# Kernel tuning notes

Measured on AMD Instinct MI355X. Metric: run time of the kernel, lower is better.

## Reference

```python
import jax, jax.numpy as jnp
import numpy as np

EPS = 1e-5
STEPS = 4
MULTIPLIER = 4
CROP_SHIFT = 4  # deterministic stand-in for RandomCrop: translate by 4px


def _box_blur(x):
    # 3x3 box blur, reflect padding (kornia RandomBoxBlur default), shape-preserving
    H, W = x.shape[-2], x.shape[-1]
    xp = jnp.pad(x, ((0, 0), (0, 0), (1, 1), (1, 1)), mode='reflect')
    acc = xp[..., 0:H, 0:W]
    for i in range(3):
        for j in range(3):
            if i == 0 and j == 0:
                continue
            acc = acc + xp[..., i:i + H, j:j + W]
    return acc / 9.0


def _mixed_op(h, w):
    # weighted sum over the 7 DA_2D_PRIMITIVES (deterministic versions):
    # none, blur, invert, hflip, vflip, crop(translate), rotate(90 deg)
    return (w[0] * h
            + w[1] * _box_blur(h)
            + w[2] * (1.0 - h)
            + w[3] * jnp.flip(h, axis=-1)
            + w[4] * jnp.flip(h, axis=-2)
            + w[5] * jnp.roll(h, shift=(CROP_SHIFT, CROP_SHIFT), axis=(-2, -1))
            + w[6] * jnp.rot90(h, k=1, axes=(-2, -1)))


def _cell(s0, s1, weights):
    states = [s0, s1]
    offset = 0
    for i in range(STEPS):
        s = states[0] * 0.0
        for j, h in enumerate(states):
            s = s + _mixed_op(h, weights[offset + j])
        offset += len(states)
        states.append(s)
    return jnp.concatenate(states[-MULTIPLIER:], axis=1)


def setup_inputs() -> dict:
    key = jax.random.key(0)
    k1, k2, k3 = jax.random.split(key, 3)
    B, C, H, W = 16, 48, 128, 128
    return {
        'x': jax.random.normal(k1, (B, C, H, W), dtype=jnp.float32),
        'gamma': jnp.ones((C,), dtype=jnp.float32),
        'beta': jnp.zeros((C,), dtype=jnp.float32),
        'alphas_normal': 0.001 * jax.random.normal(k2, (14, 7), dtype=jnp.float32),
        'alphas_reduce': 0.001 * jax.random.normal(k3, (14, 7), dtype=jnp.float32),
    }


def reference(x, gamma, beta, alphas_normal, alphas_reduce):
    # stem: BatchNorm2d in training mode (batch statistics)
    mean = jnp.mean(x, axis=(0, 2, 3), keepdims=True)
    var = jnp.var(x, axis=(0, 2, 3), keepdims=True)
    s = (x - mean) * jax.lax.rsqrt(var + EPS)
    s = s * gamma[None, :, None, None] + beta[None, :, None, None]
    # layers=1: cell 0 is a reduction cell -> uses alphas_reduce
    w = jax.nn.softmax(alphas_reduce, axis=-1)  # [14 edges, 7 ops]
    return _cell(s, s, w)
```

## Files before the change

### kernel.cpp

```cpp
#include <hip/hip_runtime.h>
#include <math.h>

#define NCH 48
#define NB 16
#define PLANE 16384
#define NPLANES 768

#define WS_PSUM  0
#define WS_PSQ   768
#define WS_SCALE 1536
#define WS_SHIFT 1584
#define WS_TAB   1632
#define WS_CONST 1728

typedef _Float16 h2 __attribute__((ext_vector_type(2)));

__global__ __launch_bounds__(256) void stats_kernel(const float* __restrict__ x,
                                                    float* __restrict__ ws) {
  int p = blockIdx.x;
  int t = threadIdx.x;
  const float4* x4 = (const float4*)x + (size_t)p * 4096;
  float s = 0.f, q = 0.f;
  #pragma unroll
  for (int k = 0; k < 16; ++k) {
    float4 v = x4[k * 256 + t];
    s += v.x + v.y + v.z + v.w;
    q += v.x * v.x + v.y * v.y + v.z * v.z + v.w * v.w;
  }
  #pragma unroll
  for (int off = 32; off > 0; off >>= 1) {
    s += __shfl_xor(s, off, 64);
    q += __shfl_xor(q, off, 64);
  }
  __shared__ float red[8];
  int wid = t >> 6, lane = t & 63;
  if (lane == 0) { red[wid] = s; red[4 + wid] = q; }
  __syncthreads();
  if (t == 0) {
    ws[WS_PSUM + p] = red[0] + red[1] + red[2] + red[3];
    ws[WS_PSQ  + p] = red[4] + red[5] + red[6] + red[7];
  }
}

__global__ void prep_kernel(const float* __restrict__ gamma, const float* __restrict__ beta,
                            const float* __restrict__ alphas, float* __restrict__ ws) {
  int t = threadIdx.x;
  if (t < NCH) {
    float s = 0.f, q = 0.f;
    for (int b = 0; b < NB; ++b) {
      s += ws[WS_PSUM + b * NCH + t];
      q += ws[WS_PSQ  + b * NCH + t];
    }
    const float inv = 1.0f / ((float)NB * PLANE);
    float mean = s * inv;
    float var  = q * inv - mean * mean;
    float sc = gamma[t] * rsqrtf(var + 1e-5f);
    ws[WS_SCALE + t] = sc;
    ws[WS_SHIFT + t] = beta[t] - mean * sc;
  }
  if (t == 0) {
    float w[14][7];
    for (int r = 0; r < 14; ++r) {
      float m = -1e30f;
      for (int k = 0; k < 7; ++k) m = fmaxf(m, alphas[r * 7 + k]);
      float sum = 0.f;
      for (int k = 0; k < 7; ++k) { float e = expf(alphas[r * 7 + k] - m); w[r][k] = e; sum += e; }
      float is = 1.0f / sum;
      for (int k = 0; k < 7; ++k) w[r][k] *= is;
    }
    for (int i = 0; i < 96; ++i) ws[WS_TAB + i] = 0.f;
    for (int i = 0; i < 4;  ++i) ws[WS_CONST + i] = 0.f;
    const int map[14][2] = {
      {0,0},{0,0},
      {0,1},{0,1},{1,1},
      {0,2},{0,2},{1,2},{2,2},
      {0,3},{0,3},{1,3},{2,3},{3,3}
    };
    for (int r = 0; r < 14; ++r) {
      int p = map[r][0], tg = map[r][1];
      float* cf = ws + WS_TAB + (p * 4 + tg) * 6;
      cf[0] += w[r][0] - w[r][2];
      cf[1] += w[r][1] * (1.0f / 9.0f);
      cf[2] += w[r][3];
      cf[3] += w[r][4];
      cf[4] += w[r][5];
      cf[5] += w[r][6];
      ws[WS_CONST + tg] += w[r][2];
    }
  }
}


__device__ __forceinline__ float ldshw(const h2* L, int i, int j) {
  int q = ((j >> 2) & 31) ^ (i >> 2);
  h2 p = L[(i << 6) + ((j & 2) << 4) + q];
  return (j & 1) ? (float)p.y : (float)p.x;
}

#define RDQ(L, I, B, M) {                                                      \
  int q_ = (B) ^ ((I) >> 2);                                                   \
  h2 p0_ = (L)[((I) << 6) + q_];                                               \
  h2 p1_ = (L)[((I) << 6) + 32 + q_];                                          \
  M.x = (float)p0_.x; M.y = (float)p0_.y;                                      \
  M.z = (float)p1_.x; M.w = (float)p1_.y; }

#define WRQ(L, I, B, V) {                                                      \
  int q_ = (B) ^ ((I) >> 2);                                                   \
  h2 p0_, p1_;                                                                 \
  p0_.x = (_Float16)V.x; p0_.y = (_Float16)V.y;                                \
  p1_.x = (_Float16)V.z; p1_.y = (_Float16)V.w;                                \
  (L)[((I) << 6) + q_] = p0_;                                                  \
  (L)[((I) << 6) + 32 + q_] = p1_; }

#define HROW(h, m, lo, hi)                                                     \
  h.x = lo + m.x + m.y; h.y = m.x + m.y + m.z;                                 \
  h.z = m.y + m.z + m.w; h.w = m.z + m.w + hi;

#define FMA4(T, C, M)                                                          \
  T.x += (C) * M.x; T.y += (C) * M.y; T.z += (C) * M.z; T.w += (C) * M.w;

#define BLUR4(T, A, B, Cq)                                                     \
  T.x += c1 * (A.x + B.x + Cq.x); T.y += c1 * (A.y + B.y + Cq.y);              \
  T.z += c1 * (A.z + B.z + Cq.z); T.w += c1 * (A.w + B.w + Cq.w);

#define FLIPL(T, M)                                                            \
  T.x += c2 * M.w; T.y += c2 * M.z; T.z += c2 * M.y; T.w += c2 * M.x;

#define GATHER(L, OI, TYC) {                                                   \
  float4 m, hA, hB, hC; float lo, hi; int ri;                                  \
  ri = ((OI) == 0) ? 1 : (OI) - 1;                                             \
  RDQ(L, ri, tx, m) lo = ldshw(L, ri, cLo); hi = ldshw(L, ri, cHi);            \
  HROW(hA, m, lo, hi)                                                          \
  RDQ(L, (OI), tx, m) lo = ldshw(L, (OI), cLo); hi = ldshw(L, (OI), cHi);      \
  FMA4(T0, c0, m)                                                              \
  HROW(hB, m, lo, hi)                                                          \
  RDQ(L, (OI)+1, tx, m) lo = ldshw(L, (OI)+1, cLo); hi = ldshw(L, (OI)+1, cHi);\
  FMA4(T1, c0, m)                                                              \
  HROW(hC, m, lo, hi)                                                          \
  BLUR4(T0, hA, hB, hC)                                                        \
  RDQ(L, (OI)+2, tx, m) lo = ldshw(L, (OI)+2, cLo); hi = ldshw(L, (OI)+2, cHi);\
  FMA4(T1, 0.0f, m)                                            \
  FMA4(T2, c0, m)                                                              \
  HROW(hA, m, lo, hi)                                                          \
  BLUR4(T1, hB, hC, hA)                                                        \
  RDQ(L, (OI)+3, tx, m) lo = ldshw(L, (OI)+3, cLo); hi = ldshw(L, (OI)+3, cHi);\
  FMA4(T3, c0, m)                                                              \
  HROW(hB, m, lo, hi)                                                          \
  BLUR4(T2, hC, hA, hB)                                                        \
  ri = ((OI) == 124) ? 126 : (OI) + 4;                                         \
  RDQ(L, ri, tx, m) lo = ldshw(L, ri, cLo); hi = ldshw(L, ri, cHi);            \
  HROW(hC, m, lo, hi)                                                          \
  BLUR4(T3, hA, hB, hC)                                                        \
                                                                   \
  RDQ(L, (OI),   31 - tx, m) FLIPL(T0, m)                                      \
  RDQ(L, (OI)+1, 31 - tx, m) FLIPL(T1, m)                                      \
  RDQ(L, (OI)+2, 31 - tx, m) FLIPL(T2, m)                                      \
  RDQ(L, (OI)+3, 31 - tx, m) FLIPL(T3, m)                                      \
                                                                   \
  RDQ(L, 127 - (OI), tx, m) FMA4(T0, c3, m)                                    \
  RDQ(L, 126 - (OI), tx, m) FMA4(T1, c3, m)                                    \
  RDQ(L, 125 - (OI), tx, m) FMA4(T2, c3, m)                                    \
  RDQ(L, 124 - (OI), tx, m) FMA4(T3, c3, m)                                    \
                                                              \
  RDQ(L, ((OI) - 4) & 127, rc, m) FMA4(T0, c4, m)                              \
  RDQ(L, ((OI) - 3) & 127, rc, m) FMA4(T1, c4, m)                              \
  RDQ(L, ((OI) - 2) & 127, rc, m) FMA4(T2, c4, m)                              \
  RDQ(L, ((OI) - 1) & 127, rc, m) FMA4(T3, c4, m)                              \
                                     \
  RDQ(L, oj,     31 - (TYC), m)                                                \
  T0.x += c5 * m.w; T1.x += c5 * m.z; T2.x += c5 * m.y; T3.x += c5 * m.x;      \
  RDQ(L, oj + 1, 31 - (TYC), m)                                                \
  T0.y += c5 * m.w; T1.y += c5 * m.z; T2.y += c5 * m.y; T3.y += c5 * m.x;      \
  RDQ(L, oj + 2, 31 - (TYC), m)                                                \
  T0.z += c5 * m.w; T1.z += c5 * m.z; T2.z += c5 * m.y; T3.z += c5 * m.x;      \
  RDQ(L, oj + 3, 31 - (TYC), m)                                                \
  T0.w += c5 * m.w; T1.w += c5 * m.z; T2.w += c5 * m.y; T3.w += c5 * m.x;      \
}

#define LDCF(P, TG) {                                                          \
  const float* cfp = wsf + WS_TAB + ((P) * 4 + (TG)) * 6;                      \
  c0 = cfp[0]; c1 = cfp[1]; c2 = cfp[2]; c3 = cfp[3]; c4 = cfp[4]; c5 = cfp[5]; }

#define SETC(K) {                                                              \
  float cst = wsf[WS_CONST + (K)];                                             \
  T0.x = cst; T0.y = cst; T0.z = cst; T0.w = cst; T1 = T0; T2 = T0; T3 = T0; }

#define STAGE_BN(L, OI) {                                                      \
  float4 v;                                                                    \
  v = x4[((OI)+0)*32 + tx]; v.x = v.x*sc+sh; v.y = v.y*sc+sh; v.z = v.z*sc+sh; \
  v.w = v.w*sc+sh; WRQ(L, (OI)+0, tx, v)                                       \
  v = x4[((OI)+1)*32 + tx]; v.x = v.x*sc+sh; v.y = v.y*sc+sh; v.z = v.z*sc+sh; \
  v.w = v.w*sc+sh; WRQ(L, (OI)+1, tx, v)                                       \
  v = x4[((OI)+2)*32 + tx]; v.x = v.x*sc+sh; v.y = v.y*sc+sh; v.z = v.z*sc+sh; \
  v.w = v.w*sc+sh; WRQ(L, (OI)+2, tx, v)                                       \
  v = x4[((OI)+3)*32 + tx]; v.x = v.x*sc+sh; v.y = v.y*sc+sh; v.z = v.z*sc+sh; \
  v.w = v.w*sc+sh; WRQ(L, (OI)+3, tx, v) }

#define STAGE_OUT(L, TG, OI) {                                                 \
  float4 v;                                                                    \
  v = out4[(pbase + (TG)*NCH)*4096 + ((OI)+0)*32 + tx]; WRQ(L, (OI)+0, tx, v)  \
  v = out4[(pbase + (TG)*NCH)*4096 + ((OI)+1)*32 + tx]; WRQ(L, (OI)+1, tx, v)  \
  v = out4[(pbase + (TG)*NCH)*4096 + ((OI)+2)*32 + tx]; WRQ(L, (OI)+2, tx, v)  \
  v = out4[(pbase + (TG)*NCH)*4096 + ((OI)+3)*32 + tx]; WRQ(L, (OI)+3, tx, v) }

#define WRITEV(TG, OI) {                                                       \
  out4[(pbase + (TG)*NCH)*4096 + ((OI)+0)*32 + tx] = T0;                       \
  out4[(pbase + (TG)*NCH)*4096 + ((OI)+1)*32 + tx] = T1;                       \
  out4[(pbase + (TG)*NCH)*4096 + ((OI)+2)*32 + tx] = T2;                       \
  out4[(pbase + (TG)*NCH)*4096 + ((OI)+3)*32 + tx] = T3; }

#define LOADV(TG, OI) {                                                        \
  T0 = out4[(pbase + (TG)*NCH)*4096 + ((OI)+0)*32 + tx];                       \
  T1 = out4[(pbase + (TG)*NCH)*4096 + ((OI)+1)*32 + tx];                       \
  T2 = out4[(pbase + (TG)*NCH)*4096 + ((OI)+2)*32 + tx];                       \
  T3 = out4[(pbase + (TG)*NCH)*4096 + ((OI)+3)*32 + tx]; }

#define STASHV(L, OI) {                                                        \
  WRQ(L, (OI)+0, tx, T0) WRQ(L, (OI)+1, tx, T1)                                \
  WRQ(L, (OI)+2, tx, T2) WRQ(L, (OI)+3, tx, T3) }

__global__ __launch_bounds__(256, 1)
void main_kernel(const float* __restrict__ x,
                 const float* __restrict__ wsf, float* out)
{
  __shared__ h2 lds[2 * 8192];
  h2* h0 = lds;
  h2* h1 = lds + 8192;
  int bx = blockIdx.x;
  int b = bx / NCH, c = bx % NCH;
  int tid = threadIdx.x;
  int ty = tid >> 5, tx = tid & 31;
  int oj = tx << 2;
  int cLo = (tx == 0)  ? 1   : oj - 1;
  int cHi = (tx == 31) ? 126 : oj + 4;
  int rc  = (tx + 31) & 31;
  float4* out4 = (float4*)out;
  const size_t pbase = (size_t)b * 192 + c;
  const float4* x4 = (const float4*)x + (size_t)bx * 4096;
  float sc = wsf[WS_SCALE + c], sh = wsf[WS_SHIFT + c];

  float4 T0, T1, T2, T3;
  float c0, c1, c2, c3, c4, c5;

  #pragma unroll 1
  for (int k = 0; k < 4; ++k) {
    int oi = (ty + 8 * k) << 2;
    STAGE_BN(h0, oi);
  }
  __syncthreads();

  #pragma unroll 1
  for (int k = 0; k < 4; ++k) {
    int oi = (ty + 8 * k) << 2; int tyc = ty + 8 * k;
    SETC(0); LDCF(0, 0);
    GATHER(h0, oi, tyc);
    WRITEV(0, oi);
    STASHV(h1, oi);
  }
  __syncthreads();

  #pragma unroll 1
  for (int k = 0; k < 4; ++k) {
    int oi = (ty + 8 * k) << 2; int tyc = ty + 8 * k;
    SETC(1); LDCF(0, 1); GATHER(h0, oi, tyc);
             LDCF(1, 1); GATHER(h1, oi, tyc);
    WRITEV(1, oi);
    SETC(2); LDCF(0, 2); GATHER(h0, oi, tyc);
             LDCF(1, 2); GATHER(h1, oi, tyc);
    WRITEV(2, oi);
    SETC(3); LDCF(0, 3); GATHER(h0, oi, tyc);
             LDCF(1, 3); GATHER(h1, oi, tyc);
    WRITEV(3, oi);
  }
  __syncthreads();

  #pragma unroll 1
  for (int k = 0; k < 4; ++k) {
    int oi = (ty + 8 * k) << 2;
    STAGE_OUT(h0, 1, oi);
  }
  __syncthreads();

  #pragma unroll 1
  for (int k = 0; k < 4; ++k) {
    int oi = (ty + 8 * k) << 2; int tyc = ty + 8 * k;
    LOADV(2, oi); LDCF(2, 2); GATHER(h0, oi, tyc); WRITEV(2, oi);
    STASHV(h1, oi);
  }
  __syncthreads();

  #pragma unroll 1
  for (int k = 0; k < 4; ++k) {
    int oi = (ty + 8 * k) << 2; int tyc = ty + 8 * k;
    LOADV(3, oi);
    LDCF(2, 3); GATHER(h0, oi, tyc);
    LDCF(3, 3); GATHER(h1, oi, tyc);
    WRITEV(3, oi);
  }
}

extern "C" void kernel_launch(void* const* d_in, const int* in_sizes, int n_in,
                              void* d_out, int out_size, void* d_ws, size_t ws_size,
                              hipStream_t stream) {
  (void)in_sizes; (void)n_in; (void)out_size; (void)ws_size;
  const float* x     = (const float*)d_in[0];
  const float* gamma = (const float*)d_in[1];
  const float* beta  = (const float*)d_in[2];
  const float* a_red = (const float*)d_in[4];
  float* ws  = (float*)d_ws;
  float* out = (float*)d_out;

  stats_kernel<<<NPLANES, 256, 0, stream>>>(x, ws);
  prep_kernel<<<1, 64, 0, stream>>>(gamma, beta, a_red, ws);
  main_kernel<<<NPLANES, 256, 0, stream>>>(x, ws, out);
}
```

Baseline: 116.6 us.

## Share LDS gathers across three target states and hoist coefficient loads out of loops

The second phase used to gather from h0 and h1 once for each of the three target states. It now gathers once per source and accumulates into three register accumulators, each with its own coefficient set. This cuts LDS reads and fp16-to-float conversions in that phase to about a third. Coefficient loads from the workspace are hoisted out of the loops, and a redundant zero-FMA is removed. The cost is much higher register pressure: 12 float4 accumulators and 36 scalar coefficients, which risks spills under launch_bounds(256,1).

```diff
diff --git a/kernel.cpp b/kernel.cpp
--- a/kernel.cpp
+++ b/kernel.cpp
@@ -104,11 +104,11 @@
   M.x = (float)p0_.x; M.y = (float)p0_.y;                                      \
   M.z = (float)p1_.x; M.w = (float)p1_.y; }
 
-#define WRQ(L, I, B, V) {                                                      \
+#define WRQ(L, I, B, VV) {                                                     \
   int q_ = (B) ^ ((I) >> 2);                                                   \
   h2 p0_, p1_;                                                                 \
-  p0_.x = (_Float16)V.x; p0_.y = (_Float16)V.y;                                \
-  p1_.x = (_Float16)V.z; p1_.y = (_Float16)V.w;                                \
+  p0_.x = (_Float16)VV.x; p0_.y = (_Float16)VV.y;                              \
+  p1_.x = (_Float16)VV.z; p1_.y = (_Float16)VV.w;                              \
   (L)[((I) << 6) + q_] = p0_;                                                  \
   (L)[((I) << 6) + 32 + q_] = p1_; }
 
@@ -116,74 +116,73 @@
   h.x = lo + m.x + m.y; h.y = m.x + m.y + m.z;                                 \
   h.z = m.y + m.z + m.w; h.w = m.z + m.w + hi;
 
-#define FMA4(T, C, M)                                                          \
-  T.x += (C) * M.x; T.y += (C) * M.y; T.z += (C) * M.z; T.w += (C) * M.w;
-
-#define BLUR4(T, A, B, Cq)                                                     \
-  T.x += c1 * (A.x + B.x + Cq.x); T.y += c1 * (A.y + B.y + Cq.y);              \
-  T.z += c1 * (A.z + B.z + Cq.z); T.w += c1 * (A.w + B.w + Cq.w);
-
-#define FLIPL(T, M)                                                            \
-  T.x += c2 * M.w; T.y += c2 * M.z; T.z += c2 * M.y; T.w += c2 * M.x;
-
-#define GATHER(L, OI, TYC) {                                                   \
+#define FMA4A(ACC, R, OP, M) ACC(R,x,OP,M.x) ACC(R,y,OP,M.y) ACC(R,z,OP,M.z) ACC(R,w,OP,M.w)
+#define FLIPLA(ACC, R, M)    ACC(R,x,2,M.w) ACC(R,y,2,M.z) ACC(R,z,2,M.y) ACC(R,w,2,M.x)
+#define BLUR4A(ACC, R, Ah, Bh, Ch)                                             \
+  ACC(R,x,1,(Ah.x+Bh.x+Ch.x)) ACC(R,y,1,(Ah.y+Bh.y+Ch.y))                      \
+  ACC(R,z,1,(Ah.z+Bh.z+Ch.z)) ACC(R,w,1,(Ah.w+Bh.w+Ch.w))
+
+#define GATHER(L, OI, TYC, ACC) {                                              \
   float4 m, hA, hB, hC; float lo, hi; int ri;                                  \
   ri = ((OI) == 0) ? 1 : (OI) - 1;                                             \
   RDQ(L, ri, tx, m) lo = ldshw(L, ri, cLo); hi = ldshw(L, ri, cHi);            \
   HROW(hA, m, lo, hi)                                                          \
   RDQ(L, (OI), tx, m) lo = ldshw(L, (OI), cLo); hi = ldshw(L, (OI), cHi);      \
-  FMA4(T0, c0, m)                                                              \
+  FMA4A(ACC, 0, 0, m)                                                          \
   HROW(hB, m, lo, hi)                                                          \
   RDQ(L, (OI)+1, tx, m) lo = ldshw(L, (OI)+1, cLo); hi = ldshw(L, (OI)+1, cHi);\
-  FMA4(T1, c0, m)                                                              \
+  FMA4A(ACC, 1, 0, m)                                                          \
   HROW(hC, m, lo, hi)                                                          \
-  BLUR4(T0, hA, hB, hC)                                                        \
+  BLUR4A(ACC, 0, hA, hB, hC)                                                   \
   RDQ(L, (OI)+2, tx, m) lo = ldshw(L, (OI)+2, cLo); hi = ldshw(L, (OI)+2, cHi);\
-  FMA4(T1, 0.0f, m)                                            \
-  FMA4(T2, c0, m)                                                              \
+  FMA4A(ACC, 2, 0, m)                                                          \
   HROW(hA, m, lo, hi)                                                          \
-  BLUR4(T1, hB, hC, hA)                                                        \
+  BLUR4A(ACC, 1, hB, hC, hA)                                                   \
   RDQ(L, (OI)+3, tx, m) lo = ldshw(L, (OI)+3, cLo); hi = ldshw(L, (OI)+3, cHi);\
-  FMA4(T3, c0, m)                                                              \
+  FMA4A(ACC, 3, 0, m)                                                          \
   HROW(hB, m, lo, hi)                                                          \
-  BLUR4(T2, hC, hA, hB)                                                        \
+  BLUR4A(ACC, 2, hC, hA, hB)                                                   \
   ri = ((OI) == 124) ? 126 : (OI) + 4;                                         \
   RDQ(L, ri, tx, m) lo = ldshw(L, ri, cLo); hi = ldshw(L, ri, cHi);            \
   HROW(hC, m, lo, hi)                                                          \
-  BLUR4(T3, hA, hB, hC)                                                        \
+  BLUR4A(ACC, 3, hA, hB, hC)                                                   \
                                                                    \
-  RDQ(L, (OI),   31 - tx, m) FLIPL(T0, m)                                      \
-  RDQ(L, (OI)+1, 31 - tx, m) FLIPL(T1, m)                                      \
-  RDQ(L, (OI)+2, 31 - tx, m) FLIPL(T2, m)                                      \
-  RDQ(L, (OI)+3, 31 - tx, m) FLIPL(T3, m)                                      \
+  RDQ(L, (OI),   31 - tx, m) FLIPLA(ACC, 0, m)                                 \
+  RDQ(L, (OI)+1, 31 - tx, m) FLIPLA(ACC, 1, m)                                 \
+  RDQ(L, (OI)+2, 31 - tx, m) FLIPLA(ACC, 2, m)                                 \
+  RDQ(L, (OI)+3, 31 - tx, m) FLIPLA(ACC, 3, m)                                 \
                                                                    \
-  RDQ(L, 127 - (OI), tx, m) FMA4(T0, c3, m)                                    \
-  RDQ(L, 126 - (OI), tx, m) FMA4(T1, c3, m)                                    \
-  RDQ(L, 125 - (OI), tx, m) FMA4(T2, c3, m)                                    \
-  RDQ(L, 124 - (OI), tx, m) FMA4(T3, c3, m)                                    \
+  RDQ(L, 127 - (OI), tx, m) FMA4A(ACC, 0, 3, m)                                \
+  RDQ(L, 126 - (OI), tx, m) FMA4A(ACC, 1, 3, m)                                \
+  RDQ(L, 125 - (OI), tx, m) FMA4A(ACC, 2, 3, m)                                \
+  RDQ(L, 124 - (OI), tx, m) FMA4A(ACC, 3, 3, m)                                \
                                                               \
-  RDQ(L, ((OI) - 4) & 127, rc, m) FMA4(T0, c4, m)                              \
-  RDQ(L, ((OI) - 3) & 127, rc, m) FMA4(T1, c4, m)                              \
-  RDQ(L, ((OI) - 2) & 127, rc, m) FMA4(T2, c4, m)                              \
-  RDQ(L, ((OI) - 1) & 127, rc, m) FMA4(T3, c4, m)                              \
+  RDQ(L, ((OI) - 4) & 127, rc, m) FMA4A(ACC, 0, 4, m)                          \
+  RDQ(L, ((OI) - 3) & 127, rc, m) FMA4A(ACC, 1, 4, m)                          \
+  RDQ(L, ((OI) - 2) & 127, rc, m) FMA4A(ACC, 2, 4, m)                          \
+  RDQ(L, ((OI) - 1) & 127, rc, m) FMA4A(ACC, 3, 4, m)                          \
                                      \
   RDQ(L, oj,     31 - (TYC), m)                                                \
-  T0.x += c5 * m.w; T1.x += c5 * m.z; T2.x += c5 * m.y; T3.x += c5 * m.x;      \
+  ACC(0,x,5,m.w) ACC(1,x,5,m.z) ACC(2,x,5,m.y) ACC(3,x,5,m.x)                  \
   RDQ(L, oj + 1, 31 - (TYC), m)                                                \
-  T0.y += c5 * m.w; T1.y += c5 * m.z; T2.y += c5 * m.y; T3.y += c5 * m.x;      \
+  ACC(0,y,5,m.w) ACC(1,y,5,m.z) ACC(2,y,5,m.y) ACC(3,y,5,m.x)                  \
   RDQ(L, oj + 2, 31 - (TYC), m)                                                \
-  T0.z += c5 * m.w; T1.z += c5 * m.z; T2.z += c5 * m.y; T3.z += c5 * m.x;      \
+  ACC(0,z,5,m.w) ACC(1,z,5,m.z) ACC(2,z,5,m.y) ACC(3,z,5,m.x)                  \
   RDQ(L, oj + 3, 31 - (TYC), m)                                                \
-  T0.w += c5 * m.w; T1.w += c5 * m.z; T2.w += c5 * m.y; T3.w += c5 * m.x;      \
-}
-
-#define LDCF(P, TG) {                                                          \
-  const float* cfp = wsf + WS_TAB + ((P) * 4 + (TG)) * 6;                      \
-  c0 = cfp[0]; c1 = cfp[1]; c2 = cfp[2]; c3 = cfp[3]; c4 = cfp[4]; c5 = cfp[5]; }
-
-#define SETC(K) {                                                              \
-  float cst = wsf[WS_CONST + (K)];                                             \
-  T0.x = cst; T0.y = cst; T0.z = cst; T0.w = cst; T1 = T0; T2 = T0; T3 = T0; }
+  ACC(0,w,5,m.w) ACC(1,w,5,m.z) ACC(2,w,5,m.y) ACC(3,w,5,m.x)                  \
+}
+
+#define ACC_T(R,Cc,OP,VAL)  T##R.Cc += cA##OP * (VAL);
+#define ACC_TB(R,Cc,OP,VAL) T##R.Cc += cB##OP * (VAL);
+#define ACC_3A(R,Cc,OP,VAL) { float v_=(VAL); T##R.Cc += cA##OP*v_; U##R.Cc += cB##OP*v_; W##R.Cc += cC##OP*v_; }
+#define ACC_3B(R,Cc,OP,VAL) { float v_=(VAL); T##R.Cc += cD##OP*v_; U##R.Cc += cE##OP*v_; W##R.Cc += cF##OP*v_; }
+
+#define LDCFS(PRE, P, TG) {                                                    \
+  const float* cfp_ = wsf + WS_TAB + ((P) * 4 + (TG)) * 6;                     \
+  PRE##0 = cfp_[0]; PRE##1 = cfp_[1]; PRE##2 = cfp_[2];                        \
+  PRE##3 = cfp_[3]; PRE##4 = cfp_[4]; PRE##5 = cfp_[5]; }
+
+#define SET4(A, VV) { A##0 = VV; A##1 = VV; A##2 = VV; A##3 = VV; }
 
 #define STAGE_BN(L, OI) {                                                      \
   float4 v;                                                                    \
@@ -203,21 +202,21 @@
   v = out4[(pbase + (TG)*NCH)*4096 + ((OI)+2)*32 + tx]; WRQ(L, (OI)+2, tx, v)  \
   v = out4[(pbase + (TG)*NCH)*4096 + ((OI)+3)*32 + tx]; WRQ(L, (OI)+3, tx, v) }
 
-#define WRITEV(TG, OI) {                                                       \
-  out4[(pbase + (TG)*NCH)*4096 + ((OI)+0)*32 + tx] = T0;                       \
-  out4[(pbase + (TG)*NCH)*4096 + ((OI)+1)*32 + tx] = T1;                       \
-  out4[(pbase + (TG)*NCH)*4096 + ((OI)+2)*32 + tx] = T2;                       \
-  out4[(pbase + (TG)*NCH)*4096 + ((OI)+3)*32 + tx] = T3; }
-
-#define LOADV(TG, OI) {                                                        \
-  T0 = out4[(pbase + (TG)*NCH)*4096 + ((OI)+0)*32 + tx];                       \
-  T1 = out4[(pbase + (TG)*NCH)*4096 + ((OI)+1)*32 + tx];                       \
-  T2 = out4[(pbase + (TG)*NCH)*4096 + ((OI)+2)*32 + tx];                       \
-  T3 = out4[(pbase + (TG)*NCH)*4096 + ((OI)+3)*32 + tx]; }
-
-#define STASHV(L, OI) {                                                        \
-  WRQ(L, (OI)+0, tx, T0) WRQ(L, (OI)+1, tx, T1)                                \
-  WRQ(L, (OI)+2, tx, T2) WRQ(L, (OI)+3, tx, T3) }
+#define WRITE4(A, TG, OI) {                                                    \
+  out4[(pbase + (TG)*NCH)*4096 + ((OI)+0)*32 + tx] = A##0;                     \
+  out4[(pbase + (TG)*NCH)*4096 + ((OI)+1)*32 + tx] = A##1;                     \
+  out4[(pbase + (TG)*NCH)*4096 + ((OI)+2)*32 + tx] = A##2;                     \
+  out4[(pbase + (TG)*NCH)*4096 + ((OI)+3)*32 + tx] = A##3; }
+
+#define LOAD4(A, TG, OI) {                                                     \
+  A##0 = out4[(pbase + (TG)*NCH)*4096 + ((OI)+0)*32 + tx];                     \
+  A##1 = out4[(pbase + (TG)*NCH)*4096 + ((OI)+1)*32 + tx];                     \
+  A##2 = out4[(pbase + (TG)*NCH)*4096 + ((OI)+2)*32 + tx];                     \
+  A##3 = out4[(pbase + (TG)*NCH)*4096 + ((OI)+3)*32 + tx]; }
+
+#define STASH4(A, L, OI) {                                                     \
+  WRQ(L, (OI)+0, tx, A##0) WRQ(L, (OI)+1, tx, A##1)                            \
+  WRQ(L, (OI)+2, tx, A##2) WRQ(L, (OI)+3, tx, A##3) }
 
 __global__ __launch_bounds__(256, 1)
 void main_kernel(const float* __restrict__ x,
@@ -239,8 +238,13 @@
   const float4* x4 = (const float4*)x + (size_t)bx * 4096;
   float sc = wsf[WS_SCALE + c], sh = wsf[WS_SHIFT + c];
 
-  float4 T0, T1, T2, T3;
-  float c0, c1, c2, c3, c4, c5;
+  float4 T0, T1, T2, T3, U0, U1, U2, U3, W0, W1, W2, W3;
+  float cA0, cA1, cA2, cA3, cA4, cA5;
+  float cB0, cB1, cB2, cB3, cB4, cB5;
+  float cC0, cC1, cC2, cC3, cC4, cC5;
+  float cD0, cD1, cD2, cD3, cD4, cD5;
+  float cE0, cE1, cE2, cE3, cE4, cE5;
+  float cF0, cF1, cF2, cF3, cF4, cF5;
 
   #pragma unroll 1
   for (int k = 0; k < 4; ++k) {
@@ -249,28 +253,38 @@
   }
   __syncthreads();
 
-  #pragma unroll 1
-  for (int k = 0; k < 4; ++k) {
-    int oi = (ty + 8 * k) << 2; int tyc = ty + 8 * k;
-    SETC(0); LDCF(0, 0);
-    GATHER(h0, oi, tyc);
-    WRITEV(0, oi);
-    STASHV(h1, oi);
-  }
-  __syncthreads();
-
-  #pragma unroll 1
-  for (int k = 0; k < 4; ++k) {
-    int oi = (ty + 8 * k) << 2; int tyc = ty + 8 * k;
-    SETC(1); LDCF(0, 1); GATHER(h0, oi, tyc);
-             LDCF(1, 1); GATHER(h1, oi, tyc);
-    WRITEV(1, oi);
-    SETC(2); LDCF(0, 2); GATHER(h0, oi, tyc);
-             LDCF(1, 2); GATHER(h1, oi, tyc);
-    WRITEV(2, oi);
-    SETC(3); LDCF(0, 3); GATHER(h0, oi, tyc);
-             LDCF(1, 3); GATHER(h1, oi, tyc);
-    WRITEV(3, oi);
+  LDCFS(cA, 0, 0)
+  {
+    float k0 = wsf[WS_CONST + 0];
+    float4 v0; v0.x = k0; v0.y = k0; v0.z = k0; v0.w = k0;
+    #pragma unroll 1
+    for (int k = 0; k < 4; ++k) {
+      int oi = (ty + 8 * k) << 2; int tyc = ty + 8 * k;
+      SET4(T, v0)
+      GATHER(h0, oi, tyc, ACC_T);
+      WRITE4(T, 0, oi)
+      STASH4(T, h1, oi)
+    }
+  }
+  __syncthreads();
+
+  LDCFS(cA, 0, 1) LDCFS(cB, 0, 2) LDCFS(cC, 0, 3)
+  LDCFS(cD, 1, 1) LDCFS(cE, 1, 2) LDCFS(cF, 1, 3)
+  {
+    float k1 = wsf[WS_CONST + 1], k2 = wsf[WS_CONST + 2], k3 = wsf[WS_CONST + 3];
+    float4 v1; v1.x = k1; v1.y = k1; v1.z = k1; v1.w = k1;
+    float4 v2; v2.x = k2; v2.y = k2; v2.z = k2; v2.w = k2;
+    float4 v3; v3.x = k3; v3.y = k3; v3.z = k3; v3.w = k3;
+    #pragma unroll 1
+    for (int k = 0; k < 4; ++k) {
+      int oi = (ty + 8 * k) << 2; int tyc = ty + 8 * k;
+      SET4(T, v1) SET4(U, v2) SET4(W, v3)
+      GATHER(h0, oi, tyc, ACC_3A);
+      GATHER(h1, oi, tyc, ACC_3B);
+      WRITE4(T, 1, oi)
+      WRITE4(U, 2, oi)
+      WRITE4(W, 3, oi)
+    }
   }
   __syncthreads();
 
@@ -281,21 +295,25 @@
   }
   __syncthreads();
 
+  LDCFS(cA, 2, 2)
   #pragma unroll 1
   for (int k = 0; k < 4; ++k) {
     int oi = (ty + 8 * k) << 2; int tyc = ty + 8 * k;
-    LOADV(2, oi); LDCF(2, 2); GATHER(h0, oi, tyc); WRITEV(2, oi);
-    STASHV(h1, oi);
-  }
-  __syncthreads();
-
+    LOAD4(T, 2, oi)
+    GATHER(h0, oi, tyc, ACC_T);
+    WRITE4(T, 2, oi)
+    STASH4(T, h1, oi)
+  }
+  __syncthreads();
+
+  LDCFS(cA, 2, 3) LDCFS(cB, 3, 3)
   #pragma unroll 1
   for (int k = 0; k < 4; ++k) {
     int oi = (ty + 8 * k) << 2; int tyc = ty + 8 * k;
-    LOADV(3, oi);
-    LDCF(2, 3); GATHER(h0, oi, tyc);
-    LDCF(3, 3); GATHER(h1, oi, tyc);
-    WRITEV(3, oi);
+    LOAD4(T, 3, oi)
+    GATHER(h0, oi, tyc, ACC_T);
+    GATHER(h1, oi, tyc, ACC_TB);
+    WRITE4(T, 3, oi)
   }
 }
 
```

Result: slower. 120.7 us (+3.5%).
